# Kernel tuning notes

Measured on AMD Instinct MI355X. Metric: run time of the kernel, lower is better.

Reference implementation:

```python
import jax, jax.numpy as jnp
import numpy as np

INFTY_APPROX = 1e+30
ROTARY_BASE = 10000.0
D_HEAD = 128


def rope(x):
    # x: [B, H, T, D]
    *_, length, width = x.shape
    half = width // 2
    positions = jnp.arange(length)[:, None].astype(x.dtype)          # [T, 1]
    dims = jnp.arange(half).astype(x.dtype)                           # [half]
    ang_freqs = jnp.power(ROTARY_BASE, -dims / half)[None, :]         # [1, half]
    radians = positions * ang_freqs                                   # [T, half]
    cos = jnp.cos(radians)[None, None].astype(x.dtype)                # [1,1,T,half]
    sin = jnp.sin(radians)[None, None].astype(x.dtype)
    even, odd = jnp.split(x, 2, axis=-1)
    r_even = even * cos - odd * sin
    r_odd = even * sin + odd * cos
    return jnp.concatenate([r_even, r_odd], axis=-1)


def setup_inputs() -> dict:
    key = jax.random.key(0)
    ks = jax.random.split(key, 5)
    B, T, M, D = 4, 2048, 1024, D_HEAD
    H = M // D
    x = jax.random.normal(ks[0], (B, T, M), dtype=jnp.float32)
    scale = M ** -0.5
    wq = jax.random.normal(ks[1], (H, M, D), dtype=jnp.float32) * scale
    wk = jax.random.normal(ks[2], (H, M, D), dtype=jnp.float32) * scale
    wv = jax.random.normal(ks[3], (H, M, D), dtype=jnp.float32) * scale
    wo = jax.random.normal(ks[4], (H, D, M), dtype=jnp.float32) * scale
    return {"x": x, "wq": wq, "wk": wk, "wv": wv, "wo": wo}


def reference(x, wq, wk, wv, wo):
    # x: [B, T, M]; w{q,k,v}: [H, M, D]; wo: [H, D, M]
    q = jnp.einsum('bim,hmd->bhid', x, wq)
    k = jnp.einsum('bim,hmd->bhid', x, wk)
    v = jnp.einsum('bim,hmd->bhid', x, wv)
    q = rope(q)
    k = rope(k)
    # NOTE: module scales BOTH q and k by d_head**-0.5 (mup-style 1/d overall)
    mult = jnp.asarray(D_HEAD ** -0.5, dtype=x.dtype)
    s = jnp.einsum('bhid,bhjd->bhij', q * mult, k * mult)
    T = s.shape[-1]
    i = jnp.arange(T)[:, None]
    j = jnp.arange(T)[None, :]
    mask = (i < j).astype(s.dtype)[None, None]  # future positions masked
    s = s - jnp.asarray(INFTY_APPROX, dtype=s.dtype) * mask
    p = jax.nn.softmax(s, axis=-1)
    o = jnp.einsum('bhij,bhjd->bhid', p, v)
    r = jnp.einsum('bhid,hdm->bim', o, wo)
    return r
```

## Files before the change

### kernel.cpp

```cpp
#include <hip/hip_runtime.h>
#include <math.h>


typedef unsigned short u16;
typedef __attribute__((ext_vector_type(8))) short short8;
typedef __attribute__((ext_vector_type(4))) float floatx4;

#define MFMA_B16(a, b, c) __builtin_amdgcn_mfma_f32_16x16x32_bf16((a), (b), (c), 0, 0, 0)

__device__ __forceinline__ void async_cp16(const void* g, void* l) {
  __builtin_amdgcn_global_load_lds(
      (const __attribute__((address_space(1))) unsigned int*)g,
      (__attribute__((address_space(3))) unsigned int*)l, 16, 0, 0);
}

__device__ __forceinline__ u16 f2bf(float f) {
  unsigned u = __float_as_uint(f);
  u += 0x7FFFu + ((u >> 16) & 1u);
  return (u16)(u >> 16);
}

__device__ __forceinline__ unsigned cvt_pk_bf16(float lo, float hi) {
  unsigned r;
  asm("v_cvt_pk_bf16_f32 %0, %1, %2" : "=v"(r) : "v"(lo), "v"(hi));
  return r;
}

__device__ __forceinline__ int swz8(int row, int chunk) { return ((chunk ^ (row & 7)) << 3); }


__global__ void conv_x(const float* __restrict__ xf, u16* __restrict__ xb) {
  int idx = (blockIdx.x * 256 + threadIdx.x) * 4;
  float4 v = *(const float4*)(xf + idx);
  ushort4 o = make_ushort4(f2bf(v.x), f2bf(v.y), f2bf(v.z), f2bf(v.w));
  *(ushort4*)(xb + idx) = o;
}

__global__ void prep_wqkv(const float* __restrict__ wq, const float* __restrict__ wk,
                          const float* __restrict__ wv, u16* __restrict__ wT) {
  __shared__ float tile[32][33];
  const float* src = (blockIdx.z == 0) ? wq : (blockIdx.z == 1) ? wk : wv;
  u16* dst = wT + (size_t)blockIdx.z * 1024 * 1024;
  int h = blockIdx.y >> 2, dt = blockIdx.y & 3;
  int m0 = blockIdx.x * 32, d0 = dt * 32;
  int tx = threadIdx.x, ty = threadIdx.y;
#pragma unroll
  for (int i = 0; i < 4; i++) {
    int r = ty + i * 8;
    tile[r][tx] = src[((size_t)h * 1024 + m0 + r) * 128 + d0 + tx];
  }
  __syncthreads();
#pragma unroll
  for (int i = 0; i < 4; i++) {
    int r = ty + i * 8;
    dst[((size_t)h * 128 + d0 + r) * 1024 + m0 + tx] = f2bf(tile[tx][r]);
  }
}

__global__ void prep_wo(const float* __restrict__ wo, u16* __restrict__ woT) {
  __shared__ float tile[32][33];
  int r0 = blockIdx.y * 32, c0 = blockIdx.x * 32;
  int tx = threadIdx.x, ty = threadIdx.y;
#pragma unroll
  for (int i = 0; i < 4; i++) {
    int r = ty + i * 8;
    tile[r][tx] = wo[(size_t)(r0 + r) * 1024 + c0 + tx];
  }
  __syncthreads();
#pragma unroll
  for (int i = 0; i < 4; i++) {
    int r = ty + i * 8;
    woT[(size_t)(c0 + r) * 1024 + r0 + tx] = f2bf(tile[tx][r]);
  }
}

__global__ void prep_rope(float2* __restrict__ tab) {
  int idx = blockIdx.x * 256 + threadIdx.x;
  int t = idx >> 6, d = idx & 63;
  const float c1 = -0.20762050593046015f;
  const float SQ = 0.10616522f;
  float freq = exp2f((float)d * c1);
  float rad = (float)t * freq;
  float s, c;
  sincosf(rad, &s, &c);
  tab[idx] = make_float2(c * SQ, s * SQ);
}

template <int MODE>
__launch_bounds__(256, 2)
__global__ void gemm_bt(const u16* __restrict__ A, const u16* __restrict__ Bt,
                        void* __restrict__ out0, u16* __restrict__ out_k,
                        u16* __restrict__ out_v, const float2* __restrict__ ropetab) {
  __shared__ u16 smem[16384];
  u16* As = smem;
  u16* Bs = smem + 8192;
  const int tid = threadIdx.x;
  const int w = tid >> 6, lane = tid & 63, quad = lane >> 4, l15 = lane & 15;
  const int row0 = blockIdx.x * 128;
  const int by = blockIdx.y;
  const int n0 = by * 128;

  floatx4 acc[2][8] = {};

  for (int kt = 0; kt < 16; ++kt) {
    __syncthreads();
#pragma unroll
    for (int i = 0; i < 4; i++) {
      int cidx = (w * 4 + i) * 64 + lane;
      int r = cidx >> 3, c = cidx & 7, cg = c ^ (r & 7);
      async_cp16(A + (size_t)(row0 + r) * 1024 + kt * 64 + cg * 8, As + (w * 4 + i) * 512);
      async_cp16(Bt + (size_t)(n0 + r) * 1024 + kt * 64 + cg * 8, Bs + (w * 4 + i) * 512);
    }
    __syncthreads();
#pragma unroll
    for (int ks = 0; ks < 2; ks++) {
      short8 af[2];
#pragma unroll
      for (int mi = 0; mi < 2; mi++) {
        int r = w * 32 + mi * 16 + l15;
        af[mi] = *(const short8*)(As + r * 64 + swz8(r, ks * 4 + quad));
      }
#pragma unroll
      for (int ni = 0; ni < 8; ni++) {
        int n = ni * 16 + l15;
        short8 bf = *(const short8*)(Bs + n * 64 + swz8(n, ks * 4 + quad));
        acc[0][ni] = MFMA_B16(af[0], bf, acc[0][ni]);
        acc[1][ni] = MFMA_B16(af[1], bf, acc[1][ni]);
      }
    }
  }
  __syncthreads();

  if (MODE == 0) {
    int sel = by >> 3, h = by & 7;
    if (sel < 2) {
      u16* dst = sel ? out_k : (u16*)out0;
#pragma unroll
      for (int mi = 0; mi < 2; mi++) {
#pragma unroll
        for (int reg = 0; reg < 4; reg++) {
          int row = row0 + w * 32 + mi * 16 + quad * 4 + reg;
          int b = row >> 11, t = row & 2047;
          u16* drow = dst + ((size_t)(b * 8 + h) * 2048 + t) * 128;
#pragma unroll
          for (int ni = 0; ni < 4; ni++) {
            int d = ni * 16 + l15;
            float2 cs = ropetab[t * 64 + d];
            float e = acc[mi][ni][reg], o = acc[mi][ni + 4][reg];
            drow[d] = f2bf(e * cs.x - o * cs.y);
            drow[d + 64] = f2bf(e * cs.y + o * cs.x);
          }
        }
      }
    } else {
#pragma unroll
      for (int mi = 0; mi < 2; mi++) {
#pragma unroll
        for (int reg = 0; reg < 4; reg++) {
          int r = w * 32 + mi * 16 + quad * 4 + reg;
#pragma unroll
          for (int ni = 0; ni < 8; ni++) {
            int col = ni * 16 + l15;
            smem[r * 128 + swz8(r, col >> 3) + (col & 7)] = f2bf(acc[mi][ni][reg]);
          }
        }
      }
      __syncthreads();
      int tl = tid & 127, dg = tid >> 7;
      int row = row0 + tl;
      int b = row >> 11, t = row & 2047;
      int tp = (t & ~31) | ((((t >> 2) & 3) << 3) | (t & 3) | ((t & 16) >> 2));
      u16* vdst = out_v + (size_t)(b * 8 + h) * 128 * 2048;
#pragma unroll
      for (int dd = 0; dd < 64; dd++) {
        int d = dg * 64 + dd;
        u16 val = smem[tl * 128 + swz8(tl, d >> 3) + (d & 7)];
        vdst[(size_t)d * 2048 + tp] = val;
      }
    }
  } else {
    float* outf = (float*)out0;
#pragma unroll
    for (int mi = 0; mi < 2; mi++) {
#pragma unroll
      for (int reg = 0; reg < 4; reg++) {
        int row = row0 + w * 32 + mi * 16 + quad * 4 + reg;
#pragma unroll
        for (int ni = 0; ni < 8; ni++) {
          outf[(size_t)row * 1024 + n0 + ni * 16 + l15] = acc[mi][ni][reg];
        }
      }
    }
  }
}

__device__ __forceinline__ void stage_kv(const u16* kb, const u16* vb, int jt,
                                         u16* Kd, u16* Vd, int w, int lane) {
#pragma unroll
  for (int i = 0; i < 4; i++) {
    int cidx = (w * 4 + i) * 64 + lane;
    int rK = cidx >> 4, cK = cidx & 15, gK = cK ^ (rK & 7);
    async_cp16(kb + (size_t)(jt * 64 + rK) * 128 + gK * 8, Kd + (w * 4 + i) * 512);
    int rV = cidx >> 3, cV = cidx & 7, gV = cV ^ (rV & 7);
    async_cp16(vb + (size_t)rV * 2048 + jt * 64 + gV * 8, Vd + (w * 4 + i) * 512);
  }
}

__launch_bounds__(256, 2)
__global__ void flash_attn(const u16* __restrict__ Q, const u16* __restrict__ Kw,
                           const u16* __restrict__ Vw, u16* __restrict__ O) {
  __shared__ u16 smem[32768];

  const int tid = threadIdx.x;
  const int w = tid >> 6, lane = tid & 63, quad = lane >> 4, l15 = lane & 15;

  const int id = (int)blockIdx.x;
  const int bh = id & 31;
  const int p = (id >> 5) & 7;
  const int qt = (id >> 8) ? (15 - p) : p;

  const u16* qb = Q + (size_t)bh * 2048 * 128;
  const u16* kb = Kw + (size_t)bh * 2048 * 128;
  const u16* vb = Vw + (size_t)bh * 128 * 2048;
  const int b = bh >> 3, h = bh & 7;

  const int iw = qt * 128 + w * 32;
  const int nj = 2 * qt + 2;

  short8 qf[2][4];
#pragma unroll
  for (int mi = 0; mi < 2; mi++) {
    int qrow = iw + mi * 16 + l15;
#pragma unroll
    for (int ks = 0; ks < 4; ks++)
      qf[mi][ks] = *(const short8*)(qb + (size_t)qrow * 128 + ks * 32 + quad * 8);
  }

  floatx4 accO[2][8] = {};
  float lsum[2] = {0.f, 0.f};

  stage_kv(kb, vb, 0, smem, smem + 16384, w, lane);

  int cur = 0;
  for (int jt = 0; jt < nj; ++jt) {
    __syncthreads();

    if (jt + 1 < nj)
      stage_kv(kb, vb, jt + 1, smem + (cur ^ 1) * 8192, smem + 16384 + (cur ^ 1) * 8192, w, lane);

    const u16* Ks = smem + cur * 8192;
    const u16* Vs = smem + 16384 + cur * 8192;
    const int j0 = jt * 64;

    if (j0 <= iw + 31) {
      const bool partial = (j0 + 63 > iw);

      floatx4 sa[4][2] = {};
      __builtin_amdgcn_s_setprio(1);
#pragma unroll
      for (int jj = 0; jj < 4; jj++) {
        const bool ok1 = (j0 + jj * 16 <= iw + 31);
        if (!ok1) continue;
        const bool ok0 = (j0 + jj * 16 <= iw + 15);
#pragma unroll
        for (int ks = 0; ks < 4; ks++) {
          int j = jj * 16 + l15;
          short8 kf = *(const short8*)(Ks + j * 128 + swz8(j, ks * 4 + quad));
          if (ok0) sa[jj][0] = MFMA_B16(kf, qf[0][ks], sa[jj][0]);
          sa[jj][1] = MFMA_B16(kf, qf[1][ks], sa[jj][1]);
        }
      }
      __builtin_amdgcn_s_setprio(0);

      unsigned pk_[2][2][4];
#pragma unroll
      for (int mi = 0; mi < 2; mi++) {
        const int ig = iw + mi * 16 + l15;
#pragma unroll
        for (int jj = 0; jj < 4; jj++) {
          float pv[4];
#pragma unroll
          for (int r = 0; r < 4; r++) {
            float s = sa[jj][mi][r];
            if (partial) {
              int jg = j0 + jj * 16 + quad * 4 + r;
              if (jg > ig) s = -1e30f;
            }
            pv[r] = exp2f(s);
            lsum[mi] += pv[r];
          }
          pk_[mi][jj >> 1][(jj & 1) * 2 + 0] = cvt_pk_bf16(pv[0], pv[1]);
          pk_[mi][jj >> 1][(jj & 1) * 2 + 1] = cvt_pk_bf16(pv[2], pv[3]);
        }
      }

      __builtin_amdgcn_s_setprio(1);
#pragma unroll
      for (int k2 = 0; k2 < 2; k2++) {
        if (k2 == 1 && j0 + 32 > iw + 31) continue;
        union {
          unsigned u[4];
          short8 s8;
        } pa[2];
#pragma unroll
        for (int mi = 0; mi < 2; mi++) {
#pragma unroll
          for (int dw = 0; dw < 4; dw++) pa[mi].u[dw] = pk_[mi][k2][dw];
        }
#pragma unroll
        for (int nt = 0; nt < 8; nt++) {
          int dr = nt * 16 + l15;
          short8 vf = *(const short8*)(Vs + dr * 64 + swz8(dr, k2 * 4 + quad));
          accO[0][nt] = MFMA_B16(pa[0].s8, vf, accO[0][nt]);
          accO[1][nt] = MFMA_B16(pa[1].s8, vf, accO[1][nt]);
        }
      }
      __builtin_amdgcn_s_setprio(0);
    }
    cur ^= 1;
  }

#pragma unroll
  for (int mi = 0; mi < 2; mi++) {
    lsum[mi] += __shfl_xor(lsum[mi], 16);
    lsum[mi] += __shfl_xor(lsum[mi], 32);
  }

#pragma unroll
  for (int mi = 0; mi < 2; mi++) {
#pragma unroll
    for (int r = 0; r < 4; r++) {
      float lr = __shfl(lsum[mi], quad * 4 + r);
      float inv = 1.0f / fmaxf(lr, 1e-30f);
      int t = iw + mi * 16 + quad * 4 + r;
#pragma unroll
      for (int nt = 0; nt < 8; nt++) {
        O[(((size_t)b * 2048 + t) * 8 + h) * 128 + nt * 16 + l15] =
            f2bf(accO[mi][nt][r] * inv);
      }
    }
  }
}

extern "C" void kernel_launch(void* const* d_in, const int* in_sizes, int n_in,
                              void* d_out, int out_size, void* d_ws, size_t ws_size,
                              hipStream_t stream) {
  const float* x = (const float*)d_in[0];
  const float* wq = (const float*)d_in[1];
  const float* wk = (const float*)d_in[2];
  const float* wv = (const float*)d_in[3];
  const float* wo = (const float*)d_in[4];
  float* out = (float*)d_out;

  char* ws = (char*)d_ws;
  const size_t SZ = 16777216;
  u16* x_bf = (u16*)(ws);
  u16* q_ws = (u16*)(ws + SZ);
  u16* k_ws = (u16*)(ws + 2 * SZ);
  u16* v_ws = (u16*)(ws + 3 * SZ);
  u16* o_ws = (u16*)(ws + 4 * SZ);
  u16* wT = (u16*)(ws + 5 * SZ);
  u16* woT = (u16*)(ws + 5 * SZ + 6291456);
  float2* tab = (float2*)(ws + 5 * SZ + 6291456 + 2097152);

  conv_x<<<8192, 256, 0, stream>>>(x, x_bf);
  prep_wqkv<<<dim3(32, 32, 3), dim3(32, 8), 0, stream>>>(wq, wk, wv, wT);
  prep_wo<<<dim3(32, 32), dim3(32, 8), 0, stream>>>(wo, woT);
  prep_rope<<<512, 256, 0, stream>>>(tab);
  gemm_bt<0><<<dim3(64, 24), 256, 0, stream>>>(x_bf, wT, q_ws, k_ws, v_ws, tab);
  flash_attn<<<512, 256, 0, stream>>>(q_ws, k_ws, v_ws, o_ws);
  gemm_bt<1><<<dim3(64, 8), 256, 0, stream>>>(o_ws, woT, out, nullptr, nullptr, nullptr);
}
```

Before: 251.6 us.

## Split long causal query tiles across blocks and merge with a combine kernel

Reworks flash attention work distribution. Each block in the first half handles a short query tile plus the first part of a long tile's KV range, and blocks in the second half handle the remainder of the long tile. Partial fp32 outputs and row sums are written to scratch buffers that alias x_bf and the output, and a new combine kernel merges them. Row sums are now computed with an MFMA against a vector of ones instead of scalar adds and shuffles. This balances per-block work, at the cost of extra partial-buffer traffic and one more kernel launch.

```diff
diff --git a/kernel.cpp b/kernel.cpp
--- a/kernel.cpp
+++ b/kernel.cpp
@@ -206,26 +206,14 @@
   }
 }
 
-__launch_bounds__(256, 2)
-__global__ void flash_attn(const u16* __restrict__ Q, const u16* __restrict__ Kw,
-                           const u16* __restrict__ Vw, u16* __restrict__ O) {
-  __shared__ u16 smem[32768];
-
-  const int tid = threadIdx.x;
-  const int w = tid >> 6, lane = tid & 63, quad = lane >> 4, l15 = lane & 15;
-
-  const int id = (int)blockIdx.x;
-  const int bh = id & 31;
-  const int p = (id >> 5) & 7;
-  const int qt = (id >> 8) ? (15 - p) : p;
-
-  const u16* qb = Q + (size_t)bh * 2048 * 128;
-  const u16* kb = Kw + (size_t)bh * 2048 * 128;
-  const u16* vb = Vw + (size_t)bh * 128 * 2048;
-  const int b = bh >> 3, h = bh & 7;
-
+__device__ __forceinline__ void attn_tile(
+    const u16* __restrict__ qb, const u16* __restrict__ kb, const u16* __restrict__ vb,
+    u16* __restrict__ O, float* __restrict__ partp, float* __restrict__ plp,
+    int qt, int jb, int je, int w, int lane, int quad, int l15,
+    u16* smem, int b, int h) {
   const int iw = qt * 128 + w * 32;
-  const int nj = 2 * qt + 2;
+
+  __syncthreads();
 
   short8 qf[2][4];
 #pragma unroll
@@ -236,16 +224,19 @@
       qf[mi][ks] = *(const short8*)(qb + (size_t)qrow * 128 + ks * 32 + quad * 8);
   }
 
+  short8 onesf;
+#pragma unroll
+  for (int i = 0; i < 8; i++) onesf[i] = (short)0x3F80;
+
   floatx4 accO[2][8] = {};
-  float lsum[2] = {0.f, 0.f};
-
-  stage_kv(kb, vb, 0, smem, smem + 16384, w, lane);
+  floatx4 accLs[2] = {};
+
+  stage_kv(kb, vb, jb, smem, smem + 16384, w, lane);
 
   int cur = 0;
-  for (int jt = 0; jt < nj; ++jt) {
+  for (int jt = jb; jt < je; ++jt) {
     __syncthreads();
-
-    if (jt + 1 < nj)
+    if (jt + 1 < je)
       stage_kv(kb, vb, jt + 1, smem + (cur ^ 1) * 8192, smem + 16384 + (cur ^ 1) * 8192, w, lane);
 
     const u16* Ks = smem + cur * 8192;
@@ -287,7 +278,6 @@
               if (jg > ig) s = -1e30f;
             }
             pv[r] = exp2f(s);
-            lsum[mi] += pv[r];
           }
           pk_[mi][jj >> 1][(jj & 1) * 2 + 0] = cvt_pk_bf16(pv[0], pv[1]);
           pk_[mi][jj >> 1][(jj & 1) * 2 + 1] = cvt_pk_bf16(pv[2], pv[3]);
@@ -307,6 +297,8 @@
 #pragma unroll
           for (int dw = 0; dw < 4; dw++) pa[mi].u[dw] = pk_[mi][k2][dw];
         }
+        accLs[0] = MFMA_B16(pa[0].s8, onesf, accLs[0]);
+        accLs[1] = MFMA_B16(pa[1].s8, onesf, accLs[1]);
 #pragma unroll
         for (int nt = 0; nt < 8; nt++) {
           int dr = nt * 16 + l15;
@@ -320,25 +312,87 @@
     cur ^= 1;
   }
 
-#pragma unroll
-  for (int mi = 0; mi < 2; mi++) {
-    lsum[mi] += __shfl_xor(lsum[mi], 16);
-    lsum[mi] += __shfl_xor(lsum[mi], 32);
-  }
-
-#pragma unroll
-  for (int mi = 0; mi < 2; mi++) {
-#pragma unroll
-    for (int r = 0; r < 4; r++) {
-      float lr = __shfl(lsum[mi], quad * 4 + r);
-      float inv = 1.0f / fmaxf(lr, 1e-30f);
-      int t = iw + mi * 16 + quad * 4 + r;
-#pragma unroll
-      for (int nt = 0; nt < 8; nt++) {
-        O[(((size_t)b * 2048 + t) * 8 + h) * 128 + nt * 16 + l15] =
-            f2bf(accO[mi][nt][r] * inv);
-      }
-    }
+  if (partp == nullptr) {
+#pragma unroll
+    for (int mi = 0; mi < 2; mi++) {
+#pragma unroll
+      for (int r = 0; r < 4; r++) {
+        float inv = 1.0f / fmaxf(accLs[mi][r], 1e-30f);
+        int t = iw + mi * 16 + quad * 4 + r;
+#pragma unroll
+        for (int nt = 0; nt < 8; nt++) {
+          O[(((size_t)b * 2048 + t) * 8 + h) * 128 + nt * 16 + l15] =
+              f2bf(accO[mi][nt][r] * inv);
+        }
+      }
+    }
+  } else {
+#pragma unroll
+    for (int mi = 0; mi < 2; mi++) {
+#pragma unroll
+      for (int r = 0; r < 4; r++) {
+        int lrow = w * 32 + mi * 16 + quad * 4 + r;
+#pragma unroll
+        for (int nt = 0; nt < 8; nt++) {
+          partp[lrow * 128 + nt * 16 + l15] = accO[mi][nt][r];
+        }
+        if (l15 == 0) plp[lrow] = accLs[mi][r];
+      }
+    }
+  }
+}
+
+__launch_bounds__(256, 2)
+__global__ void flash_attn(const u16* __restrict__ Q, const u16* __restrict__ Kw,
+                           const u16* __restrict__ Vw, u16* __restrict__ O,
+                           float* __restrict__ part0, float* __restrict__ part1,
+                           float* __restrict__ pls) {
+  __shared__ u16 smem[32768];
+
+  const int tid = threadIdx.x;
+  const int w = tid >> 6, lane = tid & 63, quad = lane >> 4, l15 = lane & 15;
+
+  const int id = (int)blockIdx.x;
+  const int half = id >> 8;
+  const int sub = id & 255;
+  const int bh = sub & 31, p = sub >> 5;
+
+  const u16* qb = Q + (size_t)bh * 2048 * 128;
+  const u16* kb = Kw + (size_t)bh * 2048 * 128;
+  const u16* vb = Vw + (size_t)bh * 128 * 2048;
+  const int b = bh >> 3, h = bh & 7;
+  const int bt = 15 - p;
+
+  if (half == 0) {
+    attn_tile(qb, kb, vb, O, nullptr, nullptr, p, 0, 2 * p + 2,
+              w, lane, quad, l15, smem, b, h);
+    attn_tile(qb, kb, vb, O, part0 + (size_t)sub * 16384, pls + (size_t)sub * 128,
+              bt, 0, 15 - 2 * p, w, lane, quad, l15, smem, b, h);
+  } else {
+    attn_tile(qb, kb, vb, O, part1 + (size_t)sub * 16384, pls + (size_t)(256 + sub) * 128,
+              bt, 15 - 2 * p, 32 - 2 * p, w, lane, quad, l15, smem, b, h);
+  }
+}
+
+__global__ void combine(const float* __restrict__ part0, const float* __restrict__ part1,
+                        const float* __restrict__ pls, u16* __restrict__ O) {
+  __shared__ float ls[128];
+  const int job = blockIdx.x;
+  const int bh = job & 31, p = job >> 5;
+  const int bt = 15 - p;
+  const int bb = bh >> 3, h = bh & 7;
+  const float* P0 = part0 + (size_t)job * 16384;
+  const float* P1 = part1 + (size_t)job * 16384;
+  if (threadIdx.x < 128) {
+    float s = pls[(size_t)job * 128 + threadIdx.x] + pls[(size_t)(256 + job) * 128 + threadIdx.x];
+    ls[threadIdx.x] = 1.0f / fmaxf(s, 1e-30f);
+  }
+  __syncthreads();
+  for (int e = threadIdx.x; e < 16384; e += 256) {
+    int row = e >> 7, col = e & 127;
+    float v = (P0[e] + P1[e]) * ls[row];
+    int t = bt * 128 + row;
+    O[(((size_t)bb * 2048 + t) * 8 + h) * 128 + col] = f2bf(v);
   }
 }
 
@@ -362,12 +416,16 @@
   u16* wT = (u16*)(ws + 5 * SZ);
   u16* woT = (u16*)(ws + 5 * SZ + 6291456);
   float2* tab = (float2*)(ws + 5 * SZ + 6291456 + 2097152);
+  float* part0 = (float*)x_bf;
+  float* part1 = (float*)out;
+  float* pls = (float*)((char*)out + 16777216);
 
   conv_x<<<8192, 256, 0, stream>>>(x, x_bf);
   prep_wqkv<<<dim3(32, 32, 3), dim3(32, 8), 0, stream>>>(wq, wk, wv, wT);
   prep_wo<<<dim3(32, 32), dim3(32, 8), 0, stream>>>(wo, woT);
   prep_rope<<<512, 256, 0, stream>>>(tab);
   gemm_bt<0><<<dim3(64, 24), 256, 0, stream>>>(x_bf, wT, q_ws, k_ws, v_ws, tab);
-  flash_attn<<<512, 256, 0, stream>>>(q_ws, k_ws, v_ws, o_ws);
+  flash_attn<<<512, 256, 0, stream>>>(q_ws, k_ws, v_ws, o_ws, part0, part1, pls);
+  combine<<<256, 256, 0, stream>>>(part0, part1, pls, o_ws);
   gemm_bt<1><<<dim3(64, 8), 256, 0, stream>>>(o_ws, woT, out, nullptr, nullptr, nullptr);
 }
```

Result: faster. 243.8 us (-3.1%).
